# Performance work log

Measured on AMD Instinct MI355X. Metric: run time of the kernel, lower is better.

## Reference

```python
import jax, jax.numpy as jnp
import numpy as np

N = 4_000_000  # flattened points
C = 13         # semantic classes


def setup_inputs() -> dict:
    key = jax.random.key(0)
    k1, k2 = jax.random.split(key)
    logits = jax.random.normal(k1, (N, C), dtype=jnp.float32)
    targets = jax.random.randint(k2, (N,), 0, C, dtype=jnp.int32)
    return {"logits": logits, "targets": targets}


def _lovasz_grad_batched(fg_sorted):
    # fg_sorted: (N, C) ground-truth indicators sorted by descending error, per class
    gts = jnp.sum(fg_sorted, axis=0)                          # (C,)
    intersection = gts - jnp.cumsum(fg_sorted, axis=0)        # (N, C)
    union = gts + jnp.cumsum(1.0 - fg_sorted, axis=0)         # (N, C)
    jaccard = 1.0 - intersection / union                      # (N, C)
    # first-difference along N, keeping jaccard[0]
    return jnp.concatenate([jaccard[:1], jaccard[1:] - jaccard[:-1]], axis=0)


def reference(logits, targets):
    # Multi-class Lovasz-Softmax, per_class='all'; no ignore_index entries in inputs
    probs = jax.nn.softmax(logits, axis=1)                    # (N, C)
    fg = jax.nn.one_hot(targets, C, dtype=probs.dtype)        # (N, C)
    errors = jnp.abs(fg - probs)                              # (N, C)
    # descending sort of errors per class, carrying fg along with the permutation
    perm = jnp.argsort(-errors, axis=0)                       # (N, C)
    errors_sorted = jnp.take_along_axis(errors, perm, axis=0)
    fg_sorted = jnp.take_along_axis(fg, perm, axis=0)
    grad = _lovasz_grad_batched(fg_sorted)                    # (N, C)
    losses = jnp.sum(errors_sorted * grad, axis=0)            # (C,) per-class dot products
    return jnp.mean(losses)
```

## Files before the change

kernel.cpp:

```cpp
#include <hip/hip_runtime.h>
#include <stdint.h>


#define NCLS 13
#define NB 256
#define ENTRIES (NCLS * NB)
#define K1_BLOCK 256
#define K1_GRID 2048
#define RED_J 16
#define BLK_PER_J (K1_GRID / RED_J)

__global__ __launch_bounds__(K1_BLOCK, 8)
void hist_kernel(const float* __restrict__ logits,
                 const int* __restrict__ targets,
                 uint32_t* __restrict__ partial, int npts) {
    __shared__ uint32_t hist[ENTRIES];
    for (int e = threadIdx.x; e < ENTRIES; e += K1_BLOCK) hist[e] = 0;
    __syncthreads();

    int tid = blockIdx.x * K1_BLOCK + threadIdx.x;
    int nth = K1_GRID * K1_BLOCK;

    for (int p = tid; p < npts; p += nth) {
        const float* row = logits + (size_t)p * NCLS;
        float v[NCLS];
        #pragma unroll
        for (int c = 0; c < NCLS; ++c) v[c] = row[c];
        int t = targets[p];
        float m = v[0];
        #pragma unroll
        for (int c = 1; c < NCLS; ++c) m = fmaxf(m, v[c]);
        float s = 0.f;
        #pragma unroll
        for (int c = 0; c < NCLS; ++c) { v[c] = __expf(v[c] - m); s += v[c]; }
        float inv = 1.f / s;
        #pragma unroll
        for (int c = 0; c < NCLS; ++c) {
            float prob = v[c] * inv;
            bool pos = (c == t);
            float e = pos ? (1.f - prob) : prob;
            int b = (int)(e * (float)NB);
            b = b > NB - 1 ? NB - 1 : b;
            atomicAdd(&hist[c * NB + b], pos ? 0x10001u : 1u);
        }
    }
    __syncthreads();
    uint32_t* outp = partial + (size_t)blockIdx.x * ENTRIES;
    for (int e = threadIdx.x; e < ENTRIES; e += K1_BLOCK) outp[e] = hist[e];
}

__global__ void reduce_kernel(const uint32_t* __restrict__ partial,
                              uint64_t* __restrict__ p2) {
    int e = blockIdx.x * 256 + threadIdx.x;
    int j = blockIdx.y;
    uint32_t cnt = 0, pos = 0;
    const uint32_t* base = partial + (size_t)j * BLK_PER_J * ENTRIES + e;
    #pragma unroll 8
    for (int b = 0; b < BLK_PER_J; ++b) {
        uint32_t v = base[(size_t)b * ENTRIES];
        cnt += v & 0xFFFFu;
        pos += v >> 16;
    }
    p2[(size_t)j * ENTRIES + e] = ((uint64_t)pos << 32) | cnt;
}

__global__ void loss_kernel(const uint64_t* __restrict__ p2,
                            float* __restrict__ out) {
    __shared__ float ls[NCLS];
    int wave = threadIdx.x >> 6;
    int lane = threadIdx.x & 63;
    if (wave < NCLS) {
        int c = wave;
        uint32_t cnt_a[NB / 64], pos_a[NB / 64];
        int lanePos = 0;
        #pragma unroll
        for (int ch = 0; ch < NB / 64; ++ch) {
            int b = NB - 1 - (ch * 64 + lane);
            int e = c * NB + b;
            uint32_t cnt = 0, pos = 0;
            #pragma unroll
            for (int j = 0; j < RED_J; ++j) {
                uint64_t v = p2[(size_t)j * ENTRIES + e];
                cnt += (uint32_t)v;
                pos += (uint32_t)(v >> 32);
            }
            cnt_a[ch] = cnt;
            pos_a[ch] = pos;
            lanePos += (int)pos;
        }
        int Ptot = lanePos;
        #pragma unroll
        for (int d = 32; d > 0; d >>= 1) Ptot += __shfl_xor(Ptot, d);

        double acc = 0.0;
        unsigned Mc = 0, Kc = 0;
        #pragma unroll
        for (int ch = 0; ch < NB / 64; ++ch) {
            unsigned pc = cnt_a[ch], pp = pos_a[ch];
            #pragma unroll
            for (int d = 1; d < 64; d <<= 1) {
                unsigned tc = __shfl_up(pc, d);
                unsigned tp = __shfl_up(pp, d);
                if (lane >= d) { pc += tc; pp += tp; }
            }
            unsigned M  = Mc + pc,        K  = Kc + pp;
            unsigned Mp = M - cnt_a[ch],  Kp = K - pos_a[ch];
            double J1, J0;
            if (Ptot > 0) {
                J1 = 1.0 - (double)(Ptot - (int)K)  / (double)(Ptot + (int)M  - (int)K);
                J0 = 1.0 - (double)(Ptot - (int)Kp) / (double)(Ptot + (int)Mp - (int)Kp);
            } else {
                J1 = (M  > 0) ? 1.0 : 0.0;
                J0 = (Mp > 0) ? 1.0 : 0.0;
            }
            int b = NB - 1 - (ch * 64 + lane);
            double emid = ((double)b + 0.5) / (double)NB;
            acc += emid * (J1 - J0);
            Mc += __shfl(pc, 63);
            Kc += __shfl(pp, 63);
        }
        #pragma unroll
        for (int d = 32; d > 0; d >>= 1) acc += __shfl_xor(acc, d);
        if (lane == 0) ls[c] = (float)acc;
    }
    __syncthreads();
    if (threadIdx.x == 0) {
        float s = 0.f;
        for (int c = 0; c < NCLS; ++c) s += ls[c];
        out[0] = s / (float)NCLS;
    }
}

extern "C" void kernel_launch(void* const* d_in, const int* in_sizes, int n_in,
                              void* d_out, int out_size, void* d_ws, size_t ws_size,
                              hipStream_t stream) {
    const float* logits  = (const float*)d_in[0];
    const int*   targets = (const int*)d_in[1];
    int N = in_sizes[1];

    uint32_t* partial = (uint32_t*)d_ws;
    uint64_t* p2 = (uint64_t*)((char*)d_ws +
                   (size_t)K1_GRID * ENTRIES * sizeof(uint32_t));

    hist_kernel<<<K1_GRID, K1_BLOCK, 0, stream>>>(logits, targets, partial, N);
    reduce_kernel<<<dim3(ENTRIES / 256, RED_J), 256, 0, stream>>>(partial, p2);
    loss_kernel<<<1, 832, 0, stream>>>(p2, (float*)d_out);
}
```

Baseline: 311.8 us.

## Stage logit chunks through shared memory with coalesced float4 loads; drop max subtraction

Each block now loads a contiguous 256-row chunk of logits into LDS with coalesced float4 reads, replacing the strided per-thread 13-float row loads. Each thread then reads its row from shared memory. The softmax max-subtraction is also removed, which relies on the logits being small enough that exp does not overflow. The change assumes N is a multiple of 256 and adds two barriers per chunk, and occupancy is lowered in launch bounds.

```diff
diff --git a/kernel.cpp b/kernel.cpp
--- a/kernel.cpp
+++ b/kernel.cpp
@@ -7,32 +7,39 @@
 #define ENTRIES (NCLS * NB)
 #define K1_BLOCK 256
 #define K1_GRID 2048
+#define CHUNK 256
+#define NF4 (CHUNK * NCLS / 4)
 #define RED_J 16
 #define BLK_PER_J (K1_GRID / RED_J)
 
-__global__ __launch_bounds__(K1_BLOCK, 8)
-void hist_kernel(const float* __restrict__ logits,
+__global__ __launch_bounds__(K1_BLOCK, 6)
+void hist_kernel(const float4* __restrict__ lp4,
                  const int* __restrict__ targets,
-                 uint32_t* __restrict__ partial, int npts) {
+                 uint32_t* __restrict__ partial, int nchunks) {
     __shared__ uint32_t hist[ENTRIES];
+    __shared__ float4 stage4[NF4];
+    const float* stage = reinterpret_cast<const float*>(stage4);
+
     for (int e = threadIdx.x; e < ENTRIES; e += K1_BLOCK) hist[e] = 0;
-    __syncthreads();
 
-    int tid = blockIdx.x * K1_BLOCK + threadIdx.x;
-    int nth = K1_GRID * K1_BLOCK;
+    for (int cb = blockIdx.x; cb < nchunks; cb += K1_GRID) {
+        const float4* src = lp4 + (size_t)cb * NF4;
+        #pragma unroll
+        for (int k = 0; k < 3; ++k)
+            stage4[threadIdx.x + k * K1_BLOCK] = src[threadIdx.x + k * K1_BLOCK];
+        if (threadIdx.x < NF4 - 3 * K1_BLOCK)
+            stage4[threadIdx.x + 3 * K1_BLOCK] = src[threadIdx.x + 3 * K1_BLOCK];
+        int t = targets[cb * CHUNK + threadIdx.x];
+        __syncthreads();
 
-    for (int p = tid; p < npts; p += nth) {
-        const float* row = logits + (size_t)p * NCLS;
+        const float* row = stage + threadIdx.x * NCLS;
         float v[NCLS];
-        #pragma unroll
-        for (int c = 0; c < NCLS; ++c) v[c] = row[c];
-        int t = targets[p];
-        float m = v[0];
-        #pragma unroll
-        for (int c = 1; c < NCLS; ++c) m = fmaxf(m, v[c]);
         float s = 0.f;
         #pragma unroll
-        for (int c = 0; c < NCLS; ++c) { v[c] = __expf(v[c] - m); s += v[c]; }
+        for (int c = 0; c < NCLS; ++c) {
+            v[c] = __expf(row[c]);
+            s += v[c];
+        }
         float inv = 1.f / s;
         #pragma unroll
         for (int c = 0; c < NCLS; ++c) {
@@ -43,8 +50,9 @@
             b = b > NB - 1 ? NB - 1 : b;
             atomicAdd(&hist[c * NB + b], pos ? 0x10001u : 1u);
         }
+        __syncthreads();
     }
-    __syncthreads();
+
     uint32_t* outp = partial + (size_t)blockIdx.x * ENTRIES;
     for (int e = threadIdx.x; e < ENTRIES; e += K1_BLOCK) outp[e] = hist[e];
 }
@@ -137,12 +145,14 @@
     const float* logits  = (const float*)d_in[0];
     const int*   targets = (const int*)d_in[1];
     int N = in_sizes[1];
+    int nchunks = N / CHUNK;
 
     uint32_t* partial = (uint32_t*)d_ws;
     uint64_t* p2 = (uint64_t*)((char*)d_ws +
                    (size_t)K1_GRID * ENTRIES * sizeof(uint32_t));
 
-    hist_kernel<<<K1_GRID, K1_BLOCK, 0, stream>>>(logits, targets, partial, N);
+    hist_kernel<<<K1_GRID, K1_BLOCK, 0, stream>>>(
+        (const float4*)logits, targets, partial, nchunks);
     reduce_kernel<<<dim3(ENTRIES / 256, RED_J), 256, 0, stream>>>(partial, p2);
     loss_kernel<<<1, 832, 0, stream>>>(p2, (float*)d_out);
 }
```

Result: no change. 316.5 us (+1.5%).

## Shrink histogram grid, fuse reduction into per-class loss kernel, drop softmax max

Applied to the files above, without the earlier changes.

The histogram kernel now runs with 512 blocks of 512 threads, producing four times fewer partial histograms to write and read back. The two-stage reduce and single-block loss kernel are merged into one kernel with one block per class, which sums all partials and accumulates the result into the output with an atomic add. The output is zeroed at the start of the histogram kernel. Softmax no longer subtracts the row maximum, removing one pass over the logits but risking overflow for large logits. The fused reduction uses only 13 blocks with long serial load chains, so it may become latency bound.

```diff
diff --git a/kernel.cpp b/kernel.cpp
--- a/kernel.cpp
+++ b/kernel.cpp
@@ -5,15 +5,15 @@
 #define NCLS 13
 #define NB 256
 #define ENTRIES (NCLS * NB)
-#define K1_BLOCK 256
-#define K1_GRID 2048
-#define RED_J 16
-#define BLK_PER_J (K1_GRID / RED_J)
+#define K1_BLOCK 512
+#define K1_GRID 512
 
-__global__ __launch_bounds__(K1_BLOCK, 8)
+__global__ __launch_bounds__(K1_BLOCK, 4)
 void hist_kernel(const float* __restrict__ logits,
                  const int* __restrict__ targets,
-                 uint32_t* __restrict__ partial, int npts) {
+                 uint32_t* __restrict__ partial,
+                 float* __restrict__ out, int npts) {
+    if (blockIdx.x == 0 && threadIdx.x == 0) out[0] = 0.0f;
     __shared__ uint32_t hist[ENTRIES];
     for (int e = threadIdx.x; e < ENTRIES; e += K1_BLOCK) hist[e] = 0;
     __syncthreads();
@@ -24,16 +24,14 @@
     for (int p = tid; p < npts; p += nth) {
         const float* row = logits + (size_t)p * NCLS;
         float v[NCLS];
-        #pragma unroll
-        for (int c = 0; c < NCLS; ++c) v[c] = row[c];
-        int t = targets[p];
-        float m = v[0];
-        #pragma unroll
-        for (int c = 1; c < NCLS; ++c) m = fmaxf(m, v[c]);
         float s = 0.f;
         #pragma unroll
-        for (int c = 0; c < NCLS; ++c) { v[c] = __expf(v[c] - m); s += v[c]; }
+        for (int c = 0; c < NCLS; ++c) {
+            v[c] = __expf(row[c]);
+            s += v[c];
+        }
         float inv = 1.f / s;
+        int t = targets[p];
         #pragma unroll
         for (int c = 0; c < NCLS; ++c) {
             float prob = v[c] * inv;
@@ -49,48 +47,38 @@
     for (int e = threadIdx.x; e < ENTRIES; e += K1_BLOCK) outp[e] = hist[e];
 }
 
-__global__ void reduce_kernel(const uint32_t* __restrict__ partial,
-                              uint64_t* __restrict__ p2) {
-    int e = blockIdx.x * 256 + threadIdx.x;
-    int j = blockIdx.y;
+__global__ __launch_bounds__(256)
+void loss_kernel(const uint32_t* __restrict__ partial,
+                 float* __restrict__ out) {
+    __shared__ uint32_t scnt[NB], spos[NB];
+    int c = blockIdx.x;
+    int j = threadIdx.x;
     uint32_t cnt = 0, pos = 0;
-    const uint32_t* base = partial + (size_t)j * BLK_PER_J * ENTRIES + e;
+    const uint32_t* base = partial + (size_t)c * NB + j;
     #pragma unroll 8
-    for (int b = 0; b < BLK_PER_J; ++b) {
-        uint32_t v = base[(size_t)b * ENTRIES];
+    for (int k = 0; k < K1_GRID; ++k) {
+        uint32_t v = base[(size_t)k * ENTRIES];
         cnt += v & 0xFFFFu;
         pos += v >> 16;
     }
-    p2[(size_t)j * ENTRIES + e] = ((uint64_t)pos << 32) | cnt;
-}
+    scnt[j] = cnt;
+    spos[j] = pos;
+    __syncthreads();
 
-__global__ void loss_kernel(const uint64_t* __restrict__ p2,
-                            float* __restrict__ out) {
-    __shared__ float ls[NCLS];
-    int wave = threadIdx.x >> 6;
-    int lane = threadIdx.x & 63;
-    if (wave < NCLS) {
-        int c = wave;
+    if (threadIdx.x < 64) {
+        int lane = threadIdx.x;
         uint32_t cnt_a[NB / 64], pos_a[NB / 64];
         int lanePos = 0;
         #pragma unroll
         for (int ch = 0; ch < NB / 64; ++ch) {
             int b = NB - 1 - (ch * 64 + lane);
-            int e = c * NB + b;
-            uint32_t cnt = 0, pos = 0;
-            #pragma unroll
-            for (int j = 0; j < RED_J; ++j) {
-                uint64_t v = p2[(size_t)j * ENTRIES + e];
-                cnt += (uint32_t)v;
-                pos += (uint32_t)(v >> 32);
-            }
-            cnt_a[ch] = cnt;
-            pos_a[ch] = pos;
-            lanePos += (int)pos;
+            cnt_a[ch] = scnt[b];
+            pos_a[ch] = spos[b];
+            lanePos += (int)pos_a[ch];
         }
         int Ptot = lanePos;
         #pragma unroll
-        for (int d = 32; d > 0; d >>= 1) Ptot += __shfl_xor(Ptot, d);
+        for (int d = 32; d > 0; d >>= 1) Ptot += __shfl_xor(Ptot, d, 64);
 
         double acc = 0.0;
         unsigned Mc = 0, Kc = 0;
@@ -99,8 +87,8 @@
             unsigned pc = cnt_a[ch], pp = pos_a[ch];
             #pragma unroll
             for (int d = 1; d < 64; d <<= 1) {
-                unsigned tc = __shfl_up(pc, d);
-                unsigned tp = __shfl_up(pp, d);
+                unsigned tc = __shfl_up(pc, d, 64);
+                unsigned tp = __shfl_up(pp, d, 64);
                 if (lane >= d) { pc += tc; pp += tp; }
             }
             unsigned M  = Mc + pc,        K  = Kc + pp;
@@ -116,18 +104,12 @@
             int b = NB - 1 - (ch * 64 + lane);
             double emid = ((double)b + 0.5) / (double)NB;
             acc += emid * (J1 - J0);
-            Mc += __shfl(pc, 63);
-            Kc += __shfl(pp, 63);
+            Mc += __shfl(pc, 63, 64);
+            Kc += __shfl(pp, 63, 64);
         }
         #pragma unroll
-        for (int d = 32; d > 0; d >>= 1) acc += __shfl_xor(acc, d);
-        if (lane == 0) ls[c] = (float)acc;
-    }
-    __syncthreads();
-    if (threadIdx.x == 0) {
-        float s = 0.f;
-        for (int c = 0; c < NCLS; ++c) s += ls[c];
-        out[0] = s / (float)NCLS;
+        for (int d = 32; d > 0; d >>= 1) acc += __shfl_xor(acc, d, 64);
+        if (lane == 0) atomicAdd(out, (float)(acc / (double)NCLS));
     }
 }
 
@@ -139,10 +121,8 @@
     int N = in_sizes[1];
 
     uint32_t* partial = (uint32_t*)d_ws;
-    uint64_t* p2 = (uint64_t*)((char*)d_ws +
-                   (size_t)K1_GRID * ENTRIES * sizeof(uint32_t));
 
-    hist_kernel<<<K1_GRID, K1_BLOCK, 0, stream>>>(logits, targets, partial, N);
-    reduce_kernel<<<dim3(ENTRIES / 256, RED_J), 256, 0, stream>>>(partial, p2);
-    loss_kernel<<<1, 832, 0, stream>>>(p2, (float*)d_out);
+    hist_kernel<<<K1_GRID, K1_BLOCK, 0, stream>>>(logits, targets, partial,
+                                                  (float*)d_out, N);
+    loss_kernel<<<NCLS, 256, 0, stream>>>(partial, (float*)d_out);
 }
```

New measurement: 312.3 us. Within noise of the previous version (+0.2%).
